# Kernel optimization log

Hardware: AMD Instinct MI355X
Metric: run time of the kernel (lower is better)

The kernel has to match this reference:

```python
import jax, jax.numpy as jnp
import numpy as np

DIM = 2048
K = 8                 # top_k
M = 16                # max_transients
BIND_FRAC = 0.15
BETA = 0.05
GAMMA = 0.9
LIFETIME = 5
B, T = 64, 256

_iu, _ju = np.triu_indices(K, k=1)   # row-major: matches torch's (ii outer, jj inner) loop order
IU = jnp.asarray(_iu, jnp.int32)
JU = jnp.asarray(_ju, jnp.int32)


def _renorm(s):
    n = jnp.sqrt(jnp.sum(jnp.abs(s) ** 2, axis=-1, keepdims=True))
    return s / jnp.maximum(n, 1e-8)


def setup_inputs() -> dict:
    key = jax.random.key(0)
    ks = jax.random.split(key, 5)
    return {
        "x": jax.random.normal(ks[0], (B, T, DIM), jnp.float32),
        "tape_re": jax.random.normal(ks[1], (DIM,), jnp.float32) / np.sqrt(DIM).astype(np.float32),
        "tape_im": jax.random.normal(ks[2], (DIM,), jnp.float32) / np.sqrt(DIM).astype(np.float32),
        "eta_param": jnp.asarray(0.1, jnp.float32),
        "torque_bias_re": jax.random.normal(ks[3], (DIM,), jnp.float32) * 0.01,
        "torque_bias_im": jax.random.normal(ks[4], (DIM,), jnp.float32) * 0.01,
    }


def _per_batch(h, s, ti, tj, mre, mim, cnt, eta, tbias):
    """One timestep for one batch element. s: [D] complex64, transients: 5 arrays of [M]."""
    c = h * s                               # Hadamard reception
    _, top_idx = jax.lax.top_k(jnp.abs(c), K)
    top_c = c[top_idx]
    tm = jnp.abs(top_c)
    ph = jnp.angle(top_c)
    # co-resonance scores for the K*(K-1)/2 pairs; torch detaches via .item()
    score = jax.lax.stop_gradient(tm[IU] * tm[JU] * jnp.cos(ph[IU] - ph[JU]))
    pos = score > 0
    n_pos = jnp.sum(pos.astype(jnp.int32))
    n_bind = jnp.maximum(1, (n_pos.astype(jnp.float32) * BIND_FRAC).astype(jnp.int32))
    sorted_desc = -jnp.sort(-jnp.where(pos, score, -jnp.inf))
    theta_idx = jnp.minimum(n_bind - 1, jnp.maximum(n_pos - 1, 0))
    theta = sorted_desc[theta_idx]
    bind = (score >= theta) & (n_pos > 0)   # theta>0 so only positive scores pass

    ci = top_idx[IU]
    cj = top_idx[JU]
    prod = s[ci] * s[cj]
    mnew = jax.lax.stop_gradient(BETA * prod / jnp.maximum(jnp.abs(prod), 1e-8))  # torch detaches via .item()

    def step(tr, inp):
        ti, tj, mre, mim, cnt = tr
        ci_p, cj_p, do, mr, mi = inp
        active = cnt > 0
        match = active & (((ti == ci_p) & (tj == cj_p)) | ((ti == cj_p) & (tj == ci_p)))
        has_match = jnp.any(match)
        midx = jnp.argmax(match)
        free = ~active
        has_free = jnp.any(free)
        fidx = jnp.argmax(free)
        refresh = do & has_match
        insert = do & (~has_match) & has_free
        cnt = jnp.where(refresh, cnt.at[midx].set(LIFETIME), cnt)
        ti = jnp.where(insert, ti.at[fidx].set(ci_p), ti)
        tj = jnp.where(insert, tj.at[fidx].set(cj_p), tj)
        mre = jnp.where(insert, mre.at[fidx].set(mr), mre)
        mim = jnp.where(insert, mim.at[fidx].set(mi), mim)
        cnt = jnp.where(insert, cnt.at[fidx].set(LIFETIME), cnt)
        return (ti, tj, mre, mim, cnt), None

    (ti, tj, mre, mim, cnt), _ = jax.lax.scan(
        step, (ti, tj, mre, mim, cnt), (ci, cj, bind, mnew.real, mnew.imag))

    # decay all transients
    mre = mre * GAMMA
    mim = mim * GAMMA
    cnt = cnt - 1
    alive = (cnt > 0) & (jnp.sqrt(mre * mre + mim * mim) > 1e-6)
    cnt = jnp.where(alive, cnt, 0)
    mre = jnp.where(alive, mre, 0.0)
    mim = jnp.where(alive, mim, 0.0)

    # augment state with transients (scatter-add to both endpoints)
    s_re = s.real.at[ti].add(0.1 * mre).at[tj].add(0.1 * mre)
    s_im = s.imag.at[ti].add(0.1 * mim).at[tj].add(0.1 * mim)
    s_aug = jax.lax.complex(s_re, s_im)

    c_aug = h * s_aug
    re_c = c_aug.real
    im_c = c_aug.imag
    res_mask = ((re_c > 1e-6) & (jnp.abs(im_c) < re_c)).astype(jnp.float32)
    tor_mask = ((re_c < -1e-6) | (jnp.abs(im_c) >= jnp.abs(re_c))).astype(jnp.float32)
    orth_mask = 1.0 - res_mask - tor_mask
    update = eta * (c_aug * (1.0 - orth_mask) + tor_mask * tbias)
    s_new = _renorm(s + update)
    return s_new, ti, tj, mre, mim, cnt


def _forward(x, tape_re, tape_im, eta_param, torque_bias_re, torque_bias_im):
    Bb, Tt, D = x.shape
    s0 = _renorm(jax.lax.complex(tape_re, tape_im)[None, :])
    s0 = jnp.broadcast_to(s0, (Bb, D))
    eta = jnp.abs(eta_param)
    tbias = jax.lax.complex(torque_bias_re, torque_bias_im)
    ti0 = jnp.zeros((Bb, M), jnp.int32)
    tj0 = jnp.zeros((Bb, M), jnp.int32)
    mre0 = jnp.zeros((Bb, M), jnp.float32)
    mim0 = jnp.zeros((Bb, M), jnp.float32)
    cnt0 = jnp.zeros((Bb, M), jnp.int32)

    step_b = jax.vmap(_per_batch, in_axes=(0, 0, 0, 0, 0, 0, 0, None, None))

    def time_step(carry, h_t):
        s, ti, tj, mre, mim, cnt = carry
        s, ti, tj, mre, mim, cnt = step_b(h_t, s, ti, tj, mre, mim, cnt, eta, tbias)
        return (s, ti, tj, mre, mim, cnt), jnp.abs(s)

    _, outs = jax.lax.scan(time_step, (s0, ti0, tj0, mre0, mim0, cnt0),
                           jnp.transpose(x, (1, 0, 2)))  # [T,B,D]
    return jnp.transpose(outs, (1, 0, 2))                # [B,T,D]


def reference(x, tape_re, tape_im, eta_param, torque_bias_re, torque_bias_im):
    return _forward(x, tape_re, tape_im, eta_param, torque_bias_re, torque_bias_im)
```

## Files before the change

kernel.cpp:

```cpp
#include <hip/hip_runtime.h>
#include <math.h>

#define DIM_ 2048
#define KTOP 8
#define MSLOT 16
#define TSTEPS 256
#define NB 64
#define NTHREADS 576
#define NWORK 512
#define EPT 4

static_assert(NWORK * EPT == DIM_, "mapping");

#define DPP0(src, ctrl, rm) __builtin_amdgcn_update_dpp(0, (src), (ctrl), (rm), 0xf, true)

__device__ __forceinline__ void ced(double &a, double &b) {
  double mx = fmax(a, b);
  b = fmin(a, b);
  a = mx;
}

__device__ __forceinline__ void sort4_desc(double k[8]) {
  ced(k[0],k[1]); ced(k[2],k[3]);
  ced(k[0],k[2]); ced(k[1],k[3]);
  ced(k[1],k[2]);
}

template <int CTRL, int RM>
__device__ __forceinline__ void merge_first4(double k[8]) {
  double b[4];
#pragma unroll
  for (int i = 0; i < 4; i++) {
    int lo = DPP0(__double2loint(k[i]), CTRL, RM);
    int hi = DPP0(__double2hiint(k[i]), CTRL, RM);
    b[i] = __hiloint2double(hi, lo);
  }
  k[4] = b[3]; k[5] = b[2]; k[6] = b[1]; k[7] = b[0];
  ced(k[0],k[4]); ced(k[1],k[5]); ced(k[2],k[6]); ced(k[3],k[7]);
  ced(k[0],k[2]); ced(k[1],k[3]); ced(k[4],k[6]); ced(k[5],k[7]);
  ced(k[0],k[1]); ced(k[2],k[3]); ced(k[4],k[5]); ced(k[6],k[7]);
}

template <int CTRL, int RM>
__device__ __forceinline__ void merge_level(double k[8]) {
  double b[8];
#pragma unroll
  for (int i = 0; i < 8; i++) {
    int lo = DPP0(__double2loint(k[i]), CTRL, RM);
    int hi = DPP0(__double2hiint(k[i]), CTRL, RM);
    b[i] = __hiloint2double(hi, lo);
  }
#pragma unroll
  for (int i = 0; i < 8; i++) k[i] = fmax(k[i], b[7 - i]);
  ced(k[0],k[4]); ced(k[1],k[5]); ced(k[2],k[6]); ced(k[3],k[7]);
  ced(k[0],k[2]); ced(k[1],k[3]); ced(k[4],k[6]); ced(k[5],k[7]);
  ced(k[0],k[1]); ced(k[2],k[3]); ced(k[4],k[5]); ced(k[6],k[7]);
}

#define FMAX_STAGE(x, ctrl, rm)                                                \
  x = fmaxf(x, __int_as_float(DPP0(__float_as_int(x), ctrl, rm)))
#define FADD_STAGE(x, ctrl, rm)                                                \
  x = x + __int_as_float(DPP0(__float_as_int(x), ctrl, rm))

__device__ __forceinline__ float wave_max_f32(float x) {
  FMAX_STAGE(x, 0x111, 0xf);
  FMAX_STAGE(x, 0x112, 0xf);
  FMAX_STAGE(x, 0x114, 0xf);
  FMAX_STAGE(x, 0x118, 0xf);
  FMAX_STAGE(x, 0x142, 0xa);
  FMAX_STAGE(x, 0x143, 0xc);
  return x;
}
__device__ __forceinline__ float wave_sum_f32(float x) {
  FADD_STAGE(x, 0x111, 0xf);
  FADD_STAGE(x, 0x112, 0xf);
  FADD_STAGE(x, 0x114, 0xf);
  FADD_STAGE(x, 0x118, 0xf);
  FADD_STAGE(x, 0x142, 0xa);
  FADD_STAGE(x, 0x143, 0xc);
  return x;
}
__device__ __forceinline__ int rl63(int v) {
  return __builtin_amdgcn_readlane(v, 63);
}

__global__ void __launch_bounds__(NTHREADS)
me_fused(const float *__restrict__ x, const float *__restrict__ tape_re,
         const float *__restrict__ tape_im, const float *__restrict__ eta_param,
         const float *__restrict__ tbias_re, const float *__restrict__ tbias_im,
         float *__restrict__ out) {
  __shared__ float4 sc4[DIM_];
  __shared__ float2 dxy[DIM_];
  __shared__ unsigned long long cand_lds[8 * KTOP];
  __shared__ float red_sh[8];

  const int tid = threadIdx.x;
  const int lane = tid & 63;
  const int wid = tid >> 6;
  const int wtid = tid - 64;
  const int b = blockIdx.x;

  const float eta = fabsf(eta_param[0]);

  float vre[EPT], vim[EPT], tbre_[EPT], tbim_[EPT];
  float hcur[EPT], hnext[EPT];
  const float *xb = x + (size_t)b * TSTEPS * DIM_;

  if (wid > 0) {
    float acc = 0.f;
#pragma unroll
    for (int j = 0; j < EPT; j++) {
      int e = wtid + NWORK * j;
      float a = tape_re[e], c2 = tape_im[e];
      vre[j] = a; vim[j] = c2;
      tbre_[j] = tbias_re[e]; tbim_[j] = tbias_im[e];
      hcur[j] = xb[e]; hnext[j] = hcur[j];
      dxy[e] = make_float2(0.f, 0.f);
      acc += a * a + c2 * c2;
    }
    float ws = wave_sum_f32(acc);
    if (lane == 63) red_sh[wid - 1] = ws;
  }

  int s_ti = 0, s_tj = 0, s_cnt = 0;
  float s_mre = 0.f, s_mim = 0.f;

  __syncthreads();

  for (int t = 0; t < TSTEPS; t++) {
    if (wid > 0) {
      double key[8];
#pragma unroll
      for (int j = 0; j < EPT; j++) {
        int e = wtid + NWORK * j;
        float h = hcur[j];
        float cr = h * vre[j], ci = h * vim[j];
        float av = sqrtf(cr * cr + ci * ci);
        key[j] = __hiloint2double(__float_as_int(av), ~e);
        sc4[e] = make_float4(h, vre[j], vim[j], 0.f);
      }
      sort4_desc(key);
      merge_first4<0x111, 0xf>(key);
      merge_level<0x112, 0xf>(key);
      merge_level<0x114, 0xf>(key);
      merge_level<0x118, 0xf>(key);
      merge_level<0x142, 0xa>(key);
      merge_level<0x143, 0xc>(key);
      if (lane == 63) {
#pragma unroll
        for (int r = 0; r < KTOP; r++)
          cand_lds[(wid - 1) * KTOP + r] =
              (unsigned long long)__double_as_longlong(key[r]);
      }
    }
    __syncthreads();

    float ivn;
    {
      float tot = (red_sh[0] + red_sh[1]) + (red_sh[2] + red_sh[3]) +
                  (red_sh[4] + red_sh[5]) + (red_sh[6] + red_sh[7]);
      ivn = 1.f / fmaxf(sqrtf(tot), 1e-8f);
    }

    float osr[EPT], osi[EPT];

    if (wid == 0) {
      double c[8];
#pragma unroll
      for (int r = 0; r < KTOP; r++) {
        unsigned long long v = (lane < 8) ? cand_lds[lane * KTOP + r] : 0ull;
        c[r] = __longlong_as_double((long long)v);
      }
      merge_level<0x111, 0xf>(c);
      merge_level<0x112, 0xf>(c);
      merge_level<0x114, 0xf>(c);
      int top[KTOP];
#pragma unroll
      for (int r = 0; r < KTOP; r++)
        top[r] = ~__builtin_amdgcn_readlane(__double2loint(c[r]), 7);

      int pi = (lane < 28) ? lane : 27;
      int ii = 0, base = 0;
      if (pi >= 7)  { ii = 1; base = 7;  }
      if (pi >= 13) { ii = 2; base = 13; }
      if (pi >= 18) { ii = 3; base = 18; }
      if (pi >= 22) { ii = 4; base = 22; }
      if (pi >= 25) { ii = 5; base = 25; }
      if (pi >= 27) { ii = 6; base = 27; }
      int jj = ii + 1 + (pi - base);
      int gi = top[0];
      if (ii == 1) gi = top[1];
      if (ii == 2) gi = top[2];
      if (ii == 3) gi = top[3];
      if (ii == 4) gi = top[4];
      if (ii == 5) gi = top[5];
      if (ii == 6) gi = top[6];
      int gj = top[1];
      if (jj == 2) gj = top[2];
      if (jj == 3) gj = top[3];
      if (jj == 4) gj = top[4];
      if (jj == 5) gj = top[5];
      if (jj == 6) gj = top[6];
      if (jj == 7) gj = top[7];

      float4 c4i = sc4[gi], c4j = sc4[gj];
      float sri = c4i.y * ivn, sii2 = c4i.z * ivn;
      float srj = c4j.y * ivn, sij = c4j.z * ivn;
      float cri = c4i.x * sri, cii = c4i.x * sii2;
      float crj = c4j.x * srj, cij = c4j.x * sij;
      float score = cri * crj + cii * cij;
      bool valid = (lane < 28);
      bool pos = valid && (score > 0.f);
      unsigned long long posmask = __ballot(pos);
      int npos = __popcll(posmask);
      float pr = sri * srj - sii2 * sij;
      float pq = sri * sij + sii2 * srj;
      float ap = fmaxf(sqrtf(pr * pr + pq * pq), 1e-8f);
      float mr = (0.05f * pr) / ap, mi = (0.05f * pq) / ap;

      unsigned long long bmask = 0ull;
      if (npos > 0) {
        int nbind = (int)((float)npos * 0.15f);
        if (nbind < 1) nbind = 1;
        float val = pos ? score : -__builtin_inff();
        float th = 0.f;
        for (int k2 = 0; k2 < nbind; ++k2) {
          float mx = wave_max_f32(val);
          th = __int_as_float(rl63(__float_as_int(mx)));
          if (k2 + 1 < nbind) {
            unsigned long long em = __ballot(val == th);
            if (lane == (int)__builtin_ctzll(em)) val = -__builtin_inff();
          }
        }
        bool bind = valid && (score >= th);
        bmask = __ballot(bind);
      }
      while (bmask) {
        int pp = (int)__builtin_ctzll(bmask);
        bmask &= bmask - 1;
        int pci = __builtin_amdgcn_readlane(gi, pp);
        int pcj = __builtin_amdgcn_readlane(gj, pp);
        int pmr = __builtin_amdgcn_readlane(__float_as_int(mr), pp);
        int pmi = __builtin_amdgcn_readlane(__float_as_int(mi), pp);
        bool isslot = (lane < MSLOT);
        bool match = isslot && (s_cnt > 0) &&
                     ((s_ti == pci && s_tj == pcj) ||
                      (s_ti == pcj && s_tj == pci));
        unsigned long long mm = __ballot(match);
        if (mm != 0ull) {
          if (lane == (int)__builtin_ctzll(mm)) s_cnt = 5;
        } else {
          unsigned long long fm = __ballot(isslot && s_cnt <= 0);
          if (fm != 0ull && lane == (int)__builtin_ctzll(fm)) {
            s_ti = pci; s_tj = pcj;
            s_mre = __int_as_float(pmr); s_mim = __int_as_float(pmi);
            s_cnt = 5;
          }
        }
      }
      if (lane < MSLOT) {
        s_mre *= 0.9f; s_mim *= 0.9f; s_cnt -= 1;
        bool alive = (s_cnt > 0) &&
                     (sqrtf(s_mre * s_mre + s_mim * s_mim) > 1e-6f);
        if (!alive) { s_cnt = 0; s_mre = 0.f; s_mim = 0.f; }
        if (s_cnt > 0) {
          atomicAdd(&dxy[s_ti].x, 0.1f * s_mre);
          atomicAdd(&dxy[s_tj].x, 0.1f * s_mre);
          atomicAdd(&dxy[s_ti].y, 0.1f * s_mim);
          atomicAdd(&dxy[s_tj].y, 0.1f * s_mim);
        }
      }
    } else {
      if (t + 1 < TSTEPS) {
        const float *xr = xb + (size_t)(t + 1) * DIM_;
#pragma unroll
        for (int j = 0; j < EPT; j++) hnext[j] = xr[wtid + NWORK * j];
      }
      if (t > 0) {
        float *op = out + ((size_t)b * TSTEPS + (t - 1)) * DIM_;
#pragma unroll
        for (int j = 0; j < EPT; j++) {
          float sr = vre[j] * ivn, si = vim[j] * ivn;
          op[wtid + NWORK * j] = sqrtf(sr * sr + si * si);
        }
      }
#pragma unroll
      for (int j = 0; j < EPT; j++) {
        float sri = vre[j] * ivn, sii2 = vim[j] * ivn;
        osr[j] = sri; osi[j] = sii2;
        float h = hcur[j];
        float car = h * sri, cai = h * sii2;
        bool res = (car > 1e-6f) && (fabsf(cai) < car);
        bool tor = (car < -1e-6f) || (fabsf(cai) >= fabsf(car));
        float m1 = (res || tor) ? 1.f : 0.f;
        float mt = tor ? 1.f : 0.f;
        float ur = eta * (car * m1 + mt * tbre_[j]);
        float ui = eta * (cai * m1 + mt * tbim_[j]);
        vre[j] = sri + ur; vim[j] = sii2 + ui;
      }
    }
    __syncthreads();

    if (wid > 0) {
      float2 dd[EPT];
#pragma unroll
      for (int j = 0; j < EPT; j++) dd[j] = dxy[wtid + NWORK * j];
      float acc2 = 0.f;
#pragma unroll
      for (int j = 0; j < EPT; j++) {
        if (dd[j].x != 0.f || dd[j].y != 0.f) {
          dxy[wtid + NWORK * j] = make_float2(0.f, 0.f);
          float ar = osr[j] + dd[j].x, ai = osi[j] + dd[j].y;
          float h = hcur[j];
          float car = h * ar, cai = h * ai;
          bool res = (car > 1e-6f) && (fabsf(cai) < car);
          bool tor = (car < -1e-6f) || (fabsf(cai) >= fabsf(car));
          float m1 = (res || tor) ? 1.f : 0.f;
          float mt = tor ? 1.f : 0.f;
          float ur = eta * (car * m1 + mt * tbre_[j]);
          float ui = eta * (cai * m1 + mt * tbim_[j]);
          vre[j] = osr[j] + ur; vim[j] = osi[j] + ui;
        }
        acc2 += vre[j] * vre[j] + vim[j] * vim[j];
      }
      float ws = wave_sum_f32(acc2);
      if (lane == 63) red_sh[wid - 1] = ws;
#pragma unroll
      for (int j = 0; j < EPT; j++) hcur[j] = hnext[j];
    }
  }

  __syncthreads();
  if (wid > 0) {
    float tot = (red_sh[0] + red_sh[1]) + (red_sh[2] + red_sh[3]) +
                (red_sh[4] + red_sh[5]) + (red_sh[6] + red_sh[7]);
    float ivnF = 1.f / fmaxf(sqrtf(tot), 1e-8f);
    float *op = out + ((size_t)b * TSTEPS + (TSTEPS - 1)) * DIM_;
#pragma unroll
    for (int j = 0; j < EPT; j++) {
      float sr = vre[j] * ivnF, si = vim[j] * ivnF;
      op[wtid + NWORK * j] = sqrtf(sr * sr + si * si);
    }
  }
}

extern "C" void kernel_launch(void *const *d_in, const int *in_sizes, int n_in,
                              void *d_out, int out_size, void *d_ws,
                              size_t ws_size, hipStream_t stream) {
  const float *x = (const float *)d_in[0];
  const float *tre = (const float *)d_in[1];
  const float *tim = (const float *)d_in[2];
  const float *eta = (const float *)d_in[3];
  const float *tbre = (const float *)d_in[4];
  const float *tbim = (const float *)d_in[5];
  float *out = (float *)d_out;
  me_fused<<<NB, NTHREADS, 0, stream>>>(x, tre, tim, eta, tbre, tbim, out);
}
```

Measured before the change: 1.081 ms.

## Replace full-wave top-k sort with threshold filter and fewer, wider worker waves

Worker count drops from 8 to 4 waves with 8 elements per thread. Each thread computes the magnitudes and per-thread maxima at the end of the previous step. The block finds the 8th-largest per-thread maximum with a float32 bitonic merge and uses it as a threshold. Only elements at or above it are appended to a shared candidate list through an atomic counter, and wave 0 merges at most 128 candidates with a depth that adapts to the count. The per-step state update moves before the first barrier, overlapping the worker update with the candidate pass. Risks include candidate overflow past the 128-entry cap on ties, an extra barrier per step, and fewer waves available to hide latency.

```diff
diff --git a/kernel.cpp b/kernel.cpp
--- a/kernel.cpp
+++ b/kernel.cpp
@@ -6,9 +6,10 @@
 #define MSLOT 16
 #define TSTEPS 256
 #define NB 64
-#define NTHREADS 576
-#define NWORK 512
-#define EPT 4
+#define NTHREADS 320
+#define NWORK 256
+#define EPT 8
+#define CCAP 128
 
 static_assert(NWORK * EPT == DIM_, "mapping");
 
@@ -20,10 +21,18 @@
   a = mx;
 }
 
-__device__ __forceinline__ void sort4_desc(double k[8]) {
-  ced(k[0],k[1]); ced(k[2],k[3]);
-  ced(k[0],k[2]); ced(k[1],k[3]);
-  ced(k[1],k[2]);
+template <int CTRL, int RM>
+__device__ __forceinline__ void merge_2to4_d(double k[8]) {
+  int lo0 = DPP0(__double2loint(k[0]), CTRL, RM);
+  int hi0 = DPP0(__double2hiint(k[0]), CTRL, RM);
+  int lo1 = DPP0(__double2loint(k[1]), CTRL, RM);
+  int hi1 = DPP0(__double2hiint(k[1]), CTRL, RM);
+  double b0 = __hiloint2double(hi0, lo0);
+  double b1 = __hiloint2double(hi1, lo1);
+  double z2 = b1, z3 = b0;
+  ced(k[0], z2); ced(k[1], z3);
+  ced(k[0], k[1]); ced(z2, z3);
+  k[2] = z2; k[3] = z3;
 }
 
 template <int CTRL, int RM>
@@ -57,6 +66,40 @@
   ced(k[0],k[1]); ced(k[2],k[3]); ced(k[4],k[5]); ced(k[6],k[7]);
 }
 
+__device__ __forceinline__ void cedf(float &a, float &b) {
+  float mx = fmaxf(a, b);
+  b = fminf(a, b);
+  a = mx;
+}
+__device__ __forceinline__ void sort4f(float k[8]) {
+  cedf(k[0],k[1]); cedf(k[2],k[3]);
+  cedf(k[0],k[2]); cedf(k[1],k[3]);
+  cedf(k[1],k[2]);
+}
+template <int CTRL, int RM>
+__device__ __forceinline__ void merge_first4_f32(float k[8]) {
+  float b[4];
+#pragma unroll
+  for (int i = 0; i < 4; i++)
+    b[i] = __int_as_float(DPP0(__float_as_int(k[i]), CTRL, RM));
+  k[4] = b[3]; k[5] = b[2]; k[6] = b[1]; k[7] = b[0];
+  cedf(k[0],k[4]); cedf(k[1],k[5]); cedf(k[2],k[6]); cedf(k[3],k[7]);
+  cedf(k[0],k[2]); cedf(k[1],k[3]); cedf(k[4],k[6]); cedf(k[5],k[7]);
+  cedf(k[0],k[1]); cedf(k[2],k[3]); cedf(k[4],k[5]); cedf(k[6],k[7]);
+}
+template <int CTRL, int RM>
+__device__ __forceinline__ void merge_level_f32(float k[8]) {
+  float b[8];
+#pragma unroll
+  for (int i = 0; i < 8; i++)
+    b[i] = __int_as_float(DPP0(__float_as_int(k[i]), CTRL, RM));
+#pragma unroll
+  for (int i = 0; i < 8; i++) k[i] = fmaxf(k[i], b[7 - i]);
+  cedf(k[0],k[4]); cedf(k[1],k[5]); cedf(k[2],k[6]); cedf(k[3],k[7]);
+  cedf(k[0],k[2]); cedf(k[1],k[3]); cedf(k[4],k[6]); cedf(k[5],k[7]);
+  cedf(k[0],k[1]); cedf(k[2],k[3]); cedf(k[4],k[5]); cedf(k[6],k[7]);
+}
+
 #define FMAX_STAGE(x, ctrl, rm)                                                \
   x = fmaxf(x, __int_as_float(DPP0(__float_as_int(x), ctrl, rm)))
 #define FADD_STAGE(x, ctrl, rm)                                                \
@@ -91,8 +134,10 @@
          float *__restrict__ out) {
   __shared__ float4 sc4[DIM_];
   __shared__ float2 dxy[DIM_];
-  __shared__ unsigned long long cand_lds[8 * KTOP];
-  __shared__ float red_sh[8];
+  __shared__ float4 lmax4[NWORK / 4];
+  __shared__ unsigned long long cand_lds[CCAP];
+  __shared__ int ccnt;
+  __shared__ float red_sh[4];
 
   const int tid = threadIdx.x;
   const int lane = tid & 63;
@@ -103,81 +148,121 @@
   const float eta = fabsf(eta_param[0]);
 
   float vre[EPT], vim[EPT], tbre_[EPT], tbim_[EPT];
-  float hcur[EPT], hnext[EPT];
+  float hcur[EPT], hnext[EPT], av[EPT];
   const float *xb = x + (size_t)b * TSTEPS * DIM_;
 
   if (wid > 0) {
-    float acc = 0.f;
+    float acc = 0.f, lm = 0.f;
 #pragma unroll
     for (int j = 0; j < EPT; j++) {
       int e = wtid + NWORK * j;
       float a = tape_re[e], c2 = tape_im[e];
       vre[j] = a; vim[j] = c2;
       tbre_[j] = tbias_re[e]; tbim_[j] = tbias_im[e];
-      hcur[j] = xb[e]; hnext[j] = hcur[j];
+      float h = xb[e];
+      hcur[j] = h; hnext[j] = h;
       dxy[e] = make_float2(0.f, 0.f);
       acc += a * a + c2 * c2;
+      float cr = h * a, ci = h * c2;
+      av[j] = sqrtf(cr * cr + ci * ci);
+      lm = fmaxf(lm, av[j]);
+      sc4[e] = make_float4(h, a, c2, 0.f);
     }
     float ws = wave_sum_f32(acc);
     if (lane == 63) red_sh[wid - 1] = ws;
+    ((float *)lmax4)[wtid] = lm;
   }
+  if (tid == 0) ccnt = 0;
 
   int s_ti = 0, s_tj = 0, s_cnt = 0;
   float s_mre = 0.f, s_mim = 0.f;
 
+  float osr[EPT], osi[EPT];
+
   __syncthreads();
 
   for (int t = 0; t < TSTEPS; t++) {
-    if (wid > 0) {
-      double key[8];
-#pragma unroll
-      for (int j = 0; j < EPT; j++) {
-        int e = wtid + NWORK * j;
-        float h = hcur[j];
-        float cr = h * vre[j], ci = h * vim[j];
-        float av = sqrtf(cr * cr + ci * ci);
-        key[j] = __hiloint2double(__float_as_int(av), ~e);
-        sc4[e] = make_float4(h, vre[j], vim[j], 0.f);
-      }
-      sort4_desc(key);
-      merge_first4<0x111, 0xf>(key);
-      merge_level<0x112, 0xf>(key);
-      merge_level<0x114, 0xf>(key);
-      merge_level<0x118, 0xf>(key);
-      merge_level<0x142, 0xa>(key);
-      merge_level<0x143, 0xc>(key);
-      if (lane == 63) {
-#pragma unroll
-        for (int r = 0; r < KTOP; r++)
-          cand_lds[(wid - 1) * KTOP + r] =
-              (unsigned long long)__double_as_longlong(key[r]);
-      }
-    }
-    __syncthreads();
-
     float ivn;
     {
-      float tot = (red_sh[0] + red_sh[1]) + (red_sh[2] + red_sh[3]) +
-                  (red_sh[4] + red_sh[5]) + (red_sh[6] + red_sh[7]);
+      float tot = (red_sh[0] + red_sh[1]) + (red_sh[2] + red_sh[3]);
       ivn = 1.f / fmaxf(sqrtf(tot), 1e-8f);
     }
 
-    float osr[EPT], osi[EPT];
+    if (wid > 0) {
+      if (t + 1 < TSTEPS) {
+        const float *xr = xb + (size_t)(t + 1) * DIM_;
+#pragma unroll
+        for (int j = 0; j < EPT; j++) hnext[j] = xr[wtid + NWORK * j];
+      }
+      if (t > 0) {
+        float *op = out + ((size_t)b * TSTEPS + (t - 1)) * DIM_;
+#pragma unroll
+        for (int j = 0; j < EPT; j++) {
+          float sr = vre[j] * ivn, si = vim[j] * ivn;
+          op[wtid + NWORK * j] = sqrtf(sr * sr + si * si);
+        }
+      }
+      float4 q = lmax4[lane];
+      float k[8];
+      k[0] = q.x; k[1] = q.y; k[2] = q.z; k[3] = q.w;
+      k[4] = 0.f; k[5] = 0.f; k[6] = 0.f; k[7] = 0.f;
+      sort4f(k);
+      merge_first4_f32<0x111, 0xf>(k);
+      merge_level_f32<0x112, 0xf>(k);
+      merge_level_f32<0x114, 0xf>(k);
+      merge_level_f32<0x118, 0xf>(k);
+      merge_level_f32<0x142, 0xa>(k);
+      merge_level_f32<0x143, 0xc>(k);
+      float th = __int_as_float(rl63(__float_as_int(k[7])));
+#pragma unroll
+      for (int j = 0; j < EPT; j++) {
+        if (av[j] >= th) {
+          int e = wtid + NWORK * j;
+          int slot = atomicAdd(&ccnt, 1);
+          if (slot < CCAP)
+            cand_lds[slot] = (unsigned long long)__double_as_longlong(
+                __hiloint2double(__float_as_int(av[j]), ~e));
+        }
+      }
+#pragma unroll
+      for (int j = 0; j < EPT; j++) {
+        float sri = vre[j] * ivn, sii2 = vim[j] * ivn;
+        osr[j] = sri; osi[j] = sii2;
+        float h = hcur[j];
+        float car = h * sri, cai = h * sii2;
+        bool res = (car > 1e-6f) && (fabsf(cai) < car);
+        bool tor = (car < -1e-6f) || (fabsf(cai) >= fabsf(car));
+        float m1 = (res || tor) ? 1.f : 0.f;
+        float mt = tor ? 1.f : 0.f;
+        float ur = eta * (car * m1 + mt * tbre_[j]);
+        float ui = eta * (cai * m1 + mt * tbim_[j]);
+        vre[j] = sri + ur; vim[j] = sii2 + ui;
+      }
+    }
+    __syncthreads();
 
     if (wid == 0) {
+      int cnt = ccnt;
+      if (lane == 0) ccnt = 0;
+      if (cnt > CCAP) cnt = CCAP;
+      unsigned long long u0 = cand_lds[2 * lane];
+      unsigned long long u1 = cand_lds[2 * lane + 1];
+      double a = (2 * lane < cnt) ? __longlong_as_double((long long)u0) : 0.0;
+      double b2 = (2 * lane + 1 < cnt) ? __longlong_as_double((long long)u1) : 0.0;
       double c[8];
-#pragma unroll
-      for (int r = 0; r < KTOP; r++) {
-        unsigned long long v = (lane < 8) ? cand_lds[lane * KTOP + r] : 0ull;
-        c[r] = __longlong_as_double((long long)v);
-      }
-      merge_level<0x111, 0xf>(c);
-      merge_level<0x112, 0xf>(c);
+      c[0] = fmax(a, b2); c[1] = fmin(a, b2);
+      c[2] = 0.0; c[3] = 0.0; c[4] = 0.0; c[5] = 0.0; c[6] = 0.0; c[7] = 0.0;
+      merge_2to4_d<0x111, 0xf>(c);
+      merge_first4<0x112, 0xf>(c);
       merge_level<0x114, 0xf>(c);
+      merge_level<0x118, 0xf>(c);
+      int src = 15;
+      if (cnt > 32) { merge_level<0x142, 0xa>(c); src = 31; }
+      if (cnt > 64) { merge_level<0x143, 0xc>(c); src = 63; }
       int top[KTOP];
 #pragma unroll
       for (int r = 0; r < KTOP; r++)
-        top[r] = ~__builtin_amdgcn_readlane(__double2loint(c[r]), 7);
+        top[r] = ~__builtin_amdgcn_readlane(__double2loint(c[r]), src);
 
       int pi = (lane < 28) ? lane : 27;
       int ii = 0, base = 0;
@@ -223,16 +308,16 @@
         int nbind = (int)((float)npos * 0.15f);
         if (nbind < 1) nbind = 1;
         float val = pos ? score : -__builtin_inff();
-        float th = 0.f;
+        float th2 = 0.f;
         for (int k2 = 0; k2 < nbind; ++k2) {
           float mx = wave_max_f32(val);
-          th = __int_as_float(rl63(__float_as_int(mx)));
+          th2 = __int_as_float(rl63(__float_as_int(mx)));
           if (k2 + 1 < nbind) {
-            unsigned long long em = __ballot(val == th);
+            unsigned long long em = __ballot(val == th2);
             if (lane == (int)__builtin_ctzll(em)) val = -__builtin_inff();
           }
         }
-        bool bind = valid && (score >= th);
+        bool bind = valid && (score >= th2);
         bmask = __ballot(bind);
       }
       while (bmask) {
@@ -270,34 +355,6 @@
           atomicAdd(&dxy[s_tj].y, 0.1f * s_mim);
         }
       }
-    } else {
-      if (t + 1 < TSTEPS) {
-        const float *xr = xb + (size_t)(t + 1) * DIM_;
-#pragma unroll
-        for (int j = 0; j < EPT; j++) hnext[j] = xr[wtid + NWORK * j];
-      }
-      if (t > 0) {
-        float *op = out + ((size_t)b * TSTEPS + (t - 1)) * DIM_;
-#pragma unroll
-        for (int j = 0; j < EPT; j++) {
-          float sr = vre[j] * ivn, si = vim[j] * ivn;
-          op[wtid + NWORK * j] = sqrtf(sr * sr + si * si);
-        }
-      }
-#pragma unroll
-      for (int j = 0; j < EPT; j++) {
-        float sri = vre[j] * ivn, sii2 = vim[j] * ivn;
-        osr[j] = sri; osi[j] = sii2;
-        float h = hcur[j];
-        float car = h * sri, cai = h * sii2;
-        bool res = (car > 1e-6f) && (fabsf(cai) < car);
-        bool tor = (car < -1e-6f) || (fabsf(cai) >= fabsf(car));
-        float m1 = (res || tor) ? 1.f : 0.f;
-        float mt = tor ? 1.f : 0.f;
-        float ur = eta * (car * m1 + mt * tbre_[j]);
-        float ui = eta * (cai * m1 + mt * tbim_[j]);
-        vre[j] = sri + ur; vim[j] = sii2 + ui;
-      }
     }
     __syncthreads();
 
@@ -305,11 +362,12 @@
       float2 dd[EPT];
 #pragma unroll
       for (int j = 0; j < EPT; j++) dd[j] = dxy[wtid + NWORK * j];
-      float acc2 = 0.f;
+      float acc2 = 0.f, lm = 0.f;
 #pragma unroll
       for (int j = 0; j < EPT; j++) {
+        int e = wtid + NWORK * j;
         if (dd[j].x != 0.f || dd[j].y != 0.f) {
-          dxy[wtid + NWORK * j] = make_float2(0.f, 0.f);
+          dxy[e] = make_float2(0.f, 0.f);
           float ar = osr[j] + dd[j].x, ai = osi[j] + dd[j].y;
           float h = hcur[j];
           float car = h * ar, cai = h * ai;
@@ -322,18 +380,22 @@
           vre[j] = osr[j] + ur; vim[j] = osi[j] + ui;
         }
         acc2 += vre[j] * vre[j] + vim[j] * vim[j];
+        float h = hnext[j];
+        hcur[j] = h;
+        float cr = h * vre[j], ci = h * vim[j];
+        av[j] = sqrtf(cr * cr + ci * ci);
+        lm = fmaxf(lm, av[j]);
+        sc4[e] = make_float4(h, vre[j], vim[j], 0.f);
       }
       float ws = wave_sum_f32(acc2);
       if (lane == 63) red_sh[wid - 1] = ws;
-#pragma unroll
-      for (int j = 0; j < EPT; j++) hcur[j] = hnext[j];
-    }
+      ((float *)lmax4)[wtid] = lm;
+    }
+    __syncthreads();
   }
 
-  __syncthreads();
   if (wid > 0) {
-    float tot = (red_sh[0] + red_sh[1]) + (red_sh[2] + red_sh[3]) +
-                (red_sh[4] + red_sh[5]) + (red_sh[6] + red_sh[7]);
+    float tot = (red_sh[0] + red_sh[1]) + (red_sh[2] + red_sh[3]);
     float ivnF = 1.f / fmaxf(sqrtf(tot), 1e-8f);
     float *op = out + ((size_t)b * TSTEPS + (TSTEPS - 1)) * DIM_;
 #pragma unroll
```

Result: slower. 1.253 ms (+15.8%).
